# Kernel tuning notes

Hardware: AMD Instinct MI355X
Metric: run time of the kernel (lower is better)

## Reference

```python
import jax, jax.numpy as jnp
import numpy as np
import math

B, N, R = 1024, 50, 1000
N_POIS = 50000
D = 128
K_T = 64
K_D = 64
T_MAX = 10080.0
D_MAX = 200.0
EARTH_RADIUS_KM = 6371.0
DEG2RAD = math.pi / 180.0


def _interp_scalar(table, x):
    # Linear interpolation into 1-D table [K]; x are bin positions in [0, K-1].
    K = table.shape[0]
    x = jnp.clip(x, 0.0, K - 1 - 1e-06)
    k = jnp.floor(x).astype(jnp.int32)
    frac = x - k.astype(x.dtype)
    return (1.0 - frac) * table[k] + frac * table[jnp.minimum(k + 1, K - 1)]


def _haversine_km(lat1, lon1, lat2, lon2):
    dlat = (lat2 - lat1) * DEG2RAD
    dlon = (lon2 - lon1) * DEG2RAD
    a = jnp.sin(dlat / 2) ** 2 + jnp.cos(lat1 * DEG2RAD) * jnp.cos(lat2 * DEG2RAD) * jnp.sin(dlon / 2) ** 2
    a = jnp.clip(a, 0.0, 1.0)
    return EARTH_RADIUS_KM * 2.0 * jnp.arcsin(jnp.sqrt(a))


def setup_inputs() -> dict:
    key = jax.random.key(0)
    ks = jax.random.split(key, 16)
    poi_idx = jax.random.randint(ks[0], (B, N), 0, N_POIS)
    hour_of_week = jax.random.randint(ks[1], (B, N), 0, 169)
    lat = jax.random.uniform(ks[2], (B, N), jnp.float32)  # ~1 degree spread => up to ~150 km pairwise
    lon = jax.random.uniform(ks[3], (B, N), jnp.float32)
    t_min = jax.random.uniform(ks[4], (B, N), jnp.float32) * T_MAX
    region_centroids = jax.random.uniform(ks[5], (R, 2), jnp.float32)
    poi_emb = 0.02 * jax.random.normal(ks[6], (N_POIS + 1, D), jnp.float32)
    poi_emb = poi_emb.at[N_POIS].set(0.0)  # padding row
    time_emb = 0.02 * jax.random.normal(ks[7], (169, D), jnp.float32)
    time_emb = time_emb.at[0].set(0.0)  # padding row
    E_t = 0.1 * jax.random.normal(ks[8], (K_T,), jnp.float32)
    E_d = 0.1 * jax.random.normal(ks[9], (K_D,), jnp.float32)
    E_d_match = 0.1 * jax.random.normal(ks[10], (K_D,), jnp.float32)
    region_emb = 0.02 * jax.random.normal(ks[11], (R, D), jnp.float32)
    Wq = jax.random.normal(ks[12], (D, D), jnp.float32) / math.sqrt(D)
    Wk = jax.random.normal(ks[13], (D, D), jnp.float32) / math.sqrt(D)
    Wv = jax.random.normal(ks[14], (D, D), jnp.float32) / math.sqrt(D)
    return dict(poi_idx=poi_idx, hour_of_week=hour_of_week, lat=lat, lon=lon, t_min=t_min,
                region_centroids=region_centroids, poi_emb=poi_emb, time_emb=time_emb,
                E_t=E_t, E_d=E_d, E_d_match=E_d_match, region_emb=region_emb,
                Wq=Wq, Wk=Wk, Wv=Wv)


def reference(poi_idx, hour_of_week, lat, lon, t_min, region_centroids,
              poi_emb, time_emb, E_t, E_d, E_d_match, region_emb, Wq, Wk, Wv):
    pad_mask = poi_idx < 0  # [B, n]
    poi_safe = jnp.where(pad_mask, N_POIS, poi_idx)
    hour_safe = jnp.where(pad_mask, 0, hour_of_week)
    x = poi_emb[poi_safe] + time_emb[hour_safe]  # [B, n, D]

    # pairwise trajectory intervals [B, n, n]
    dt = jnp.abs(t_min[:, :, None] - t_min[:, None, :])
    dd = _haversine_km(lat[:, :, None], lon[:, :, None], lat[:, None, :], lon[:, None, :])
    valid = (~pad_mask).astype(x.dtype)
    valid_pair = valid[:, :, None] * valid[:, None, :]
    dt = dt * valid_pair
    dd = dd * valid_pair

    # _PairwiseBias: scalar table interpolation bias
    t_bin = jnp.clip(dt, 0.0, T_MAX) / T_MAX * (K_T - 1)
    d_bin = jnp.clip(dd, 0.0, D_MAX) / D_MAX * (K_D - 1)
    bias = _interp_scalar(E_t, t_bin) + _interp_scalar(E_d, d_bin)  # [B, n, n]

    # _SelfAttn (single head, no LN/residual, dropout=0)
    Q = x @ Wq.T
    K_ = x @ Wk.T
    V = x @ Wv.T
    scores = jnp.einsum('bnd,bmd->bnm', Q, K_) / math.sqrt(D) + bias
    scores = jnp.where(pad_mask[:, None, :], -jnp.inf, scores)
    attn = jnp.nan_to_num(jax.nn.softmax(scores, axis=-1), nan=0.0)
    S = attn @ V  # [B, n, D]

    # _MatchingLayer
    cand_lat = region_centroids[:, 0]
    cand_lon = region_centroids[:, 1]
    dd_m = _haversine_km(lat[:, :, None], lon[:, :, None], cand_lat[None, None, :], cand_lon[None, None, :])  # [B, n, R]
    dbin_m = jnp.clip(dd_m, 0.0, D_MAX) / D_MAX * (K_D - 1)
    bias_match = _interp_scalar(E_d_match, dbin_m)
    m_scores = jnp.einsum('bnd,rd->bnr', S, region_emb) / math.sqrt(D) + bias_match
    m_scores = jnp.where(pad_mask[:, :, None], -jnp.inf, m_scores)
    m_attn = jnp.nan_to_num(jax.nn.softmax(m_scores, axis=1), nan=0.0)  # softmax over trajectory dim
    scores_safe = jnp.where(pad_mask[:, :, None], 0.0, m_scores)
    return jnp.sum(m_attn * scores_safe, axis=1)  # [B, R]
```

## Files before the change

### kernel.cpp

```cpp
#include <hip/hip_runtime.h>
#include <hip/hip_bf16.h>
#include <math.h>

constexpr int BB    = 1024;
constexpr int NN    = 50;
constexpr int RR    = 1000;
constexpr int DD    = 128;
constexpr int NPOIS = 50000;
#define DEG2RADF  0.017453292519943295f
#define KHALF     0.008726646259971648f
#define RSQRTD    0.08838834764831845f
#define LOG2E     1.4426950408889634f
#define LN2       0.6931471805599453f
#define DBIN_C0   4013.7373f
#define DBIN_C1   668.95621f
#define TBIN_SC   0.00625f
#define PENAL     -1.0e30f

typedef __attribute__((ext_vector_type(8))) short bfrag8;
typedef __attribute__((ext_vector_type(4))) float f32x4;

__device__ __forceinline__ int swz128(int row, int k) {
    return row * 128 + ((((k) >> 3) ^ (row & 7)) << 3) + (k & 7);
}

__device__ __forceinline__ unsigned short f2bf(float x) {
    union { __hip_bfloat16 h; unsigned short u; } cv;
    cv.h = __float2bfloat16(x);
    return cv.u;
}

__device__ __forceinline__ float exp2_asm(float x) {
    float r;
    asm("v_exp_f32 %0, %1" : "=v"(r) : "v"(x));
    return r;
}

__device__ __forceinline__ float fract_asm(float x) {
    float r;
    asm("v_fract_f32 %0, %1" : "=v"(r) : "v"(x));
    return r;
}

__device__ __forceinline__ float cos_small(float x) {
    float x2 = x * x;
    return 1.0f - 0.5f * x2 + 0.041666667f * x2 * x2;
}

__global__ void prep_mg(const float* __restrict__ Wq, const float* __restrict__ Wk,
                        const float* __restrict__ Wv, const float* __restrict__ Re,
                        unsigned short* __restrict__ Mt, unsigned short* __restrict__ Gp) {
    int k = threadIdx.x;
    if (blockIdx.x < DD) {
        int c = blockIdx.x;
        float s0 = 0.f, s1 = 0.f, s2 = 0.f, s3 = 0.f;
        for (int d = 0; d < DD; d += 4) {
            s0 += Wq[(d + 0) * DD + k] * Wk[(d + 0) * DD + c];
            s1 += Wq[(d + 1) * DD + k] * Wk[(d + 1) * DD + c];
            s2 += Wq[(d + 2) * DD + k] * Wk[(d + 2) * DD + c];
            s3 += Wq[(d + 3) * DD + k] * Wk[(d + 3) * DD + c];
        }
        Mt[c * DD + k] = f2bf((s0 + s1 + s2 + s3) * (RSQRTD * LOG2E));
    } else {
        int r = blockIdx.x - DD;
        float val = 0.f;
        if (r < RR) {
            float s0 = 0.f, s1 = 0.f, s2 = 0.f, s3 = 0.f;
            for (int d = 0; d < DD; d += 4) {
                s0 += Wv[(d + 0) * DD + k] * Re[r * DD + d + 0];
                s1 += Wv[(d + 1) * DD + k] * Re[r * DD + d + 1];
                s2 += Wv[(d + 2) * DD + k] * Re[r * DD + d + 2];
                s3 += Wv[(d + 3) * DD + k] * Re[r * DD + d + 3];
            }
            val = (s0 + s1 + s2 + s3) * (RSQRTD * LOG2E);
        }
        int rt = r >> 6, widr = (r >> 4) & 3, colr = r & 15;
        int ks = k >> 5, quad = (k >> 3) & 3, k7 = k & 7;
        int lane = quad * 16 + colr;
        Gp[((((rt * 16 + widr * 4 + ks) * 64) + lane) << 3) + k7] = f2bf(val);
    }
}

__global__ __launch_bounds__(256, 4) void stan_fused(
    const int* __restrict__ poi_idx, const int* __restrict__ hourw,
    const float* __restrict__ lat, const float* __restrict__ lon,
    const float* __restrict__ tmin,
    const float* __restrict__ poi_emb, const float* __restrict__ time_emb,
    const float* __restrict__ Et_g, const float* __restrict__ Ed_g,
    const float* __restrict__ Em_g,
    const unsigned short* __restrict__ Mtb, const unsigned short* __restrict__ Gp,
    const float* __restrict__ cent, float* __restrict__ out) {
    __shared__ short xs[64 * 128];
    __shared__ union {
        short ys[64 * 128];
        short ps[64 * 64];
        short as_[64 * 128];
    } u2;
    __shared__ float2 Et2[64], Ed2[64], Em2[64];
    __shared__ float4 bnfo[64];
    __shared__ float4 bnfoM[64];
    __shared__ float  jpen[64];
    __shared__ int2   nidx[64];

    const int b = blockIdx.x, tid = threadIdx.x;
    const int wid = tid >> 6, lane = tid & 63;
    const int quad = lane >> 4, colr = lane & 15;

    if (tid < 64) {
        int kk = tid > 62 ? 62 : tid;
        float t0 = Et_g[kk] * LOG2E, t1 = Et_g[kk + 1] * LOG2E;
        float d0 = Ed_g[kk] * LOG2E, d1 = Ed_g[kk + 1] * LOG2E;
        float e0 = Em_g[kk] * LOG2E, e1 = Em_g[kk + 1] * LOG2E;
        Et2[tid] = make_float2(t0, t1 - t0);
        Ed2[tid] = make_float2(d0, d1 - d0);
        Em2[tid] = make_float2(e0, e1 - e0);
        if (tid < NN) {
            int p = poi_idx[b * NN + tid];
            int pd = (p < 0);
            float la = lat[b * NN + tid], lo = lon[b * NN + tid];
            float cs = cos_small(la * DEG2RADF);
            float pen = pd ? PENAL : 0.f;
            nidx[tid] = make_int2(pd ? NPOIS : p, pd ? 0 : hourw[b * NN + tid]);
            bnfo[tid]  = make_float4(la * KHALF, lo * KHALF, cs,
                                     tmin[b * NN + tid] * TBIN_SC);
            bnfoM[tid] = make_float4(la * KHALF, lo * KHALF, cs, pen);
            jpen[tid] = pen;
        } else {
            nidx[tid] = make_int2(NPOIS, 0);
            bnfo[tid]  = make_float4(0.f, 0.f, 1.f, 0.f);
            bnfoM[tid] = make_float4(0.f, 0.f, 1.f, PENAL);
            jpen[tid] = PENAL;
        }
    }
    __syncthreads();

    for (int idx = tid; idx < 64 * 64; idx += 256) {
        int n = idx >> 6, c2 = idx & 63;
        int2 ix = nidx[n];
        float2 pe = ((const float2*)(poi_emb  + (size_t)ix.x * DD))[c2];
        float2 te = ((const float2*)(time_emb + (size_t)ix.y * DD))[c2];
        unsigned pack = (unsigned)f2bf(pe.x + te.x)
                      | ((unsigned)f2bf(pe.y + te.y) << 16);
        ((unsigned*)xs)[n * 64 + (((c2 >> 2) ^ (n & 7)) << 2) + (c2 & 3)] = pack;
    }
    __syncthreads();

    const int q8    = (quad ^ (colr & 3)) * 8;
    const int kx    = (colr & 4) * 8;
    const int xbase = colr * 128 + q8;
    const int xe = xbase + kx, xo = xbase - kx;

    {
        f32x4 accY[2][4];
        #pragma unroll
        for (int ct = 0; ct < 2; ct++)
            #pragma unroll
            for (int mt = 0; mt < 4; mt++) accY[ct][mt] = (f32x4){0.f, 0.f, 0.f, 0.f};
        #pragma unroll
        for (int ks = 0; ks < 4; ks++) {
            const int k0 = ks * 32 + quad * 8;
            const int xoff = ((ks & 1) ? xo : xe) + ks * 32;
            bfrag8 av[4], bv[2];
            #pragma unroll
            for (int mt = 0; mt < 4; mt++)
                av[mt] = *(const bfrag8*)(&xs[xoff + mt * 2048]);
            #pragma unroll
            for (int ct = 0; ct < 2; ct++) {
                int c = wid * 32 + ct * 16 + colr;
                bv[ct] = *(const bfrag8*)(Mtb + (size_t)c * DD + k0);
            }
            #pragma unroll
            for (int ct = 0; ct < 2; ct++)
                #pragma unroll
                for (int mt = 0; mt < 4; mt++)
                    accY[ct][mt] = __builtin_amdgcn_mfma_f32_16x16x32_bf16(
                        av[mt], bv[ct], accY[ct][mt], 0, 0, 0);
        }
        #pragma unroll
        for (int ct = 0; ct < 2; ct++)
            #pragma unroll
            for (int mt = 0; mt < 4; mt++)
                #pragma unroll
                for (int reg = 0; reg < 4; reg++) {
                    int m = mt * 16 + quad * 4 + reg;
                    int c = wid * 32 + ct * 16 + colr;
                    u2.ys[swz128(m, c)] = (short)f2bf(accY[ct][mt][reg]);
                }
    }
    __syncthreads();

    const int i = wid * 16 + colr;
    const int ybase = xbase + wid * 2048;
    const int ye = ybase + kx, yo = ybase - kx;
    f32x4 accS[4];
    #pragma unroll
    for (int mt = 0; mt < 4; mt++) accS[mt] = (f32x4){0.f, 0.f, 0.f, 0.f};
    #pragma unroll
    for (int ks = 0; ks < 4; ks++) {
        const int yoff = ((ks & 1) ? yo : ye) + ks * 32;
        const int xoff = ((ks & 1) ? xo : xe) + ks * 32;
        bfrag8 bv = *(const bfrag8*)(&u2.ys[yoff]);
        #pragma unroll
        for (int mt = 0; mt < 4; mt++) {
            bfrag8 av = *(const bfrag8*)(&xs[xoff + mt * 2048]);
            accS[mt] = __builtin_amdgcn_mfma_f32_16x16x32_bf16(
                av, bv, accS[mt], 0, 0, 0);
        }
    }
    __syncthreads();

    {
        const float4 bi = bnfo[i];
        float sv[14];
        #pragma unroll
        for (int mt = 0; mt < 4; mt++) {
            const int nregs = (mt == 3) ? 2 : 4;
            #pragma unroll
            for (int reg = 0; reg < nregs; reg++) {
                int j = mt * 16 + quad * 4 + reg;
                float4 bj = bnfo[j];
                float tb = fabsf(bi.w - bj.w);
                int   kt = (int)tb;
                float ft = fract_asm(tb);
                float2 et = Et2[kt];
                float bt = fmaf(ft, et.y, et.x);
                float du = bi.x - bj.x, dv = bi.y - bj.y;
                float a = fmaf((bi.z * bj.z) * dv, dv, du * du);
                float x = __builtin_amdgcn_sqrtf(a);
                float db = x * fmaf(a, DBIN_C1, DBIN_C0);
                int   kd = (int)db;
                float fd = fract_asm(db);
                float2 ed = Ed2[kd];
                float bd = fmaf(fd, ed.y, ed.x);
                sv[mt * 4 + reg] = (accS[mt][reg] + bt) + (bd + jpen[j]);
            }
        }
        float l = 0.f;
        #pragma unroll
        for (int t = 0; t < 14; t++) {
            float p = exp2_asm(sv[t]);
            sv[t] = p;
            l += p;
        }
        l += __shfl_xor(l, 16, 64);
        l += __shfl_xor(l, 32, 64);
        float rl = __builtin_amdgcn_rcpf(l);
        #pragma unroll
        for (int mt = 0; mt < 4; mt++)
            #pragma unroll
            for (int rp = 0; rp < 2; rp++) {
                int j0 = mt * 16 + quad * 4 + rp * 2;
                unsigned pack;
                if (mt == 3 && rp == 1) {
                    pack = 0u;
                } else {
                    unsigned lo = f2bf(sv[mt * 4 + rp * 2]     * rl);
                    unsigned hi = f2bf(sv[mt * 4 + rp * 2 + 1] * rl);
                    pack = lo | (hi << 16);
                }
                ((unsigned*)u2.ps)[i * 32 + (((j0 >> 3) ^ (i & 7)) << 2) + ((j0 & 7) >> 1)]
                    = pack;
            }
    }
    __syncthreads();

    {
        f32x4 accZ[2][4];
        #pragma unroll
        for (int nt = 0; nt < 2; nt++)
            #pragma unroll
            for (int mt = 0; mt < 4; mt++) accZ[nt][mt] = (f32x4){0.f, 0.f, 0.f, 0.f};
        union BF { unsigned u[4]; bfrag8 v; };
        const int pbase = colr * 64 + q8;
        const int pe = pbase + kx, po = pbase - kx;
        #pragma unroll
        for (int ks = 0; ks < 2; ks++) {
            const int k0 = ks * 32 + quad * 8;
            const int poff = ((ks & 1) ? po : pe) + ks * 32;
            bfrag8 av[4];
            #pragma unroll
            for (int mt = 0; mt < 4; mt++)
                av[mt] = *(const bfrag8*)(&u2.ps[poff + mt * 1024]);
            BF bvx[2];
            #pragma unroll
            for (int nt = 0; nt < 2; nt++) {
                int d = wid * 32 + nt * 16 + colr;
                #pragma unroll
                for (int t2 = 0; t2 < 4; t2++) {
                    unsigned lo = (unsigned short)xs[swz128(k0 + 2 * t2,     d)];
                    unsigned hi = (unsigned short)xs[swz128(k0 + 2 * t2 + 1, d)];
                    bvx[nt].u[t2] = lo | (hi << 16);
                }
            }
            #pragma unroll
            for (int nt = 0; nt < 2; nt++)
                #pragma unroll
                for (int mt = 0; mt < 4; mt++)
                    accZ[nt][mt] = __builtin_amdgcn_mfma_f32_16x16x32_bf16(
                        av[mt], bvx[nt].v, accZ[nt][mt], 0, 0, 0);
        }
        __syncthreads();
        #pragma unroll
        for (int mt = 0; mt < 4; mt++)
            #pragma unroll
            for (int reg = 0; reg < 4; reg++) {
                int ii = mt * 16 + quad * 4 + reg;
                #pragma unroll
                for (int nt = 0; nt < 2; nt++) {
                    int d = wid * 32 + nt * 16 + colr;
                    float zv = (ii < NN) ? accZ[nt][mt][reg] : 0.f;
                    u2.as_[swz128(ii, d)] = (short)f2bf(zv);
                }
            }
    }
    __syncthreads();

    bfrag8 Af[4][4];
    #pragma unroll
    for (int ks = 0; ks < 4; ks++) {
        const int aoff = ((ks & 1) ? xo : xe) + ks * 32;
        #pragma unroll
        for (int mt = 0; mt < 4; mt++)
            Af[mt][ks] = *(const bfrag8*)(&u2.as_[aoff + mt * 2048]);
    }
    bfrag8 bfv[4];
    #pragma unroll
    for (int ks = 0; ks < 4; ks++)
        bfv[ks] = *(const bfrag8*)(Gp + (size_t)(((wid * 4 + ks) * 64 + lane) << 3));

    const int rL = wid * 16 + colr;

    #pragma unroll 1
    for (int it = 0; it < 16; it++) {
        f32x4 acc[4];
        #pragma unroll
        for (int mt = 0; mt < 4; mt++) acc[mt] = (f32x4){0.f, 0.f, 0.f, 0.f};
        #pragma unroll
        for (int ks = 0; ks < 4; ks++)
            #pragma unroll
            for (int mt = 0; mt < 4; mt++)
                acc[mt] = __builtin_amdgcn_mfma_f32_16x16x32_bf16(
                    Af[mt][ks], bfv[ks], acc[mt], 0, 0, 0);

        {
            const int rtn = (it < 15) ? it + 1 : it;
            #pragma unroll
            for (int ks = 0; ks < 4; ks++)
                bfv[ks] = *(const bfrag8*)(Gp + (size_t)(((rtn * 16 + wid * 4 + ks) * 64 + lane) << 3));
        }

        const int r  = it * 64 + rL;
        const int rc = (r < RR) ? r : (RR - 1);
        float2 cc = ((const float2*)cent)[rc];
        const float rvx = cc.x * KHALF, rvy = cc.y * KHALF;
        const float rvz = cos_small(cc.x * DEG2RADF);

        float l = 0.f, aw = 0.f;
        #pragma unroll
        for (int mt = 0; mt < 4; mt++) {
            const int nregs = (mt == 3) ? 2 : 4;
            #pragma unroll
            for (int reg = 0; reg < nregs; reg++) {
                int n = mt * 16 + quad * 4 + reg;
                float4 bn = bnfoM[n];
                float du = bn.x - rvx, dv = bn.y - rvy;
                float a = fmaf((bn.z * rvz) * dv, dv, du * du);
                float x = __builtin_amdgcn_sqrtf(a);
                float db = x * fmaf(a, DBIN_C1, DBIN_C0);
                int   kd = (int)db;
                float fd = fract_asm(db);
                float2 ed = Em2[kd];
                float bias = fmaf(fd, ed.y, ed.x);
                float sc = (acc[mt][reg] + bias) + bn.w;
                float p = exp2_asm(sc);
                l += p;
                aw = fmaf(p, sc, aw);
            }
        }
        l  += __shfl_xor(l, 16, 64); aw += __shfl_xor(aw, 16, 64);
        l  += __shfl_xor(l, 32, 64); aw += __shfl_xor(aw, 32, 64);
        if (quad == 0 && r < RR)
            out[(size_t)b * RR + r] = aw * __builtin_amdgcn_rcpf(l) * LN2;
    }
}

extern "C" void kernel_launch(void* const* d_in, const int* in_sizes, int n_in,
                              void* d_out, int out_size, void* d_ws, size_t ws_size,
                              hipStream_t stream) {
    const int*   poi_idx  = (const int*)d_in[0];
    const int*   hourw    = (const int*)d_in[1];
    const float* lat      = (const float*)d_in[2];
    const float* lon      = (const float*)d_in[3];
    const float* tmin     = (const float*)d_in[4];
    const float* cent     = (const float*)d_in[5];
    const float* poi_emb  = (const float*)d_in[6];
    const float* time_emb = (const float*)d_in[7];
    const float* E_t      = (const float*)d_in[8];
    const float* E_d      = (const float*)d_in[9];
    const float* E_dm     = (const float*)d_in[10];
    const float* Remb     = (const float*)d_in[11];
    const float* Wq       = (const float*)d_in[12];
    const float* Wk       = (const float*)d_in[13];
    const float* Wv       = (const float*)d_in[14];
    float* out            = (float*)d_out;

    unsigned short* Mtb = (unsigned short*)d_ws;
    unsigned short* Gpb = Mtb + DD * DD;

    prep_mg<<<dim3(DD + 1024), DD, 0, stream>>>(Wq, Wk, Wv, Remb, Mtb, Gpb);
    stan_fused<<<dim3(BB), 256, 0, stream>>>(poi_idx, hourw, lat, lon, tmin,
                                             poi_emb, time_emb, E_t, E_d, E_dm,
                                             Mtb, Gpb, cent, out);
}
```

Before: 152.4 us.

## Process two region tiles per iteration and reload A fragments from LDS

```diff
diff --git a/kernel.cpp b/kernel.cpp
--- a/kernel.cpp
+++ b/kernel.cpp
@@ -315,72 +315,76 @@
     }
     __syncthreads();
 
-    bfrag8 Af[4][4];
+    bfrag8 bf0[4], bf1[4];
     #pragma unroll
     for (int ks = 0; ks < 4; ks++) {
-        const int aoff = ((ks & 1) ? xo : xe) + ks * 32;
-        #pragma unroll
-        for (int mt = 0; mt < 4; mt++)
-            Af[mt][ks] = *(const bfrag8*)(&u2.as_[aoff + mt * 2048]);
-    }
-    bfrag8 bfv[4];
-    #pragma unroll
-    for (int ks = 0; ks < 4; ks++)
-        bfv[ks] = *(const bfrag8*)(Gp + (size_t)(((wid * 4 + ks) * 64 + lane) << 3));
+        bf0[ks] = *(const bfrag8*)(Gp + (size_t)(((      wid * 4 + ks) * 64 + lane) << 3));
+        bf1[ks] = *(const bfrag8*)(Gp + (size_t)(((16  + wid * 4 + ks) * 64 + lane) << 3));
+    }
 
     const int rL = wid * 16 + colr;
 
     #pragma unroll 1
-    for (int it = 0; it < 16; it++) {
-        f32x4 acc[4];
-        #pragma unroll
-        for (int mt = 0; mt < 4; mt++) acc[mt] = (f32x4){0.f, 0.f, 0.f, 0.f};
-        #pragma unroll
-        for (int ks = 0; ks < 4; ks++)
-            #pragma unroll
-            for (int mt = 0; mt < 4; mt++)
-                acc[mt] = __builtin_amdgcn_mfma_f32_16x16x32_bf16(
-                    Af[mt][ks], bfv[ks], acc[mt], 0, 0, 0);
-
+    for (int ot = 0; ot < 8; ot++) {
+        f32x4 acc0[4], acc1[4];
+        #pragma unroll
+        for (int mt = 0; mt < 4; mt++) {
+            acc0[mt] = (f32x4){0.f, 0.f, 0.f, 0.f};
+            acc1[mt] = (f32x4){0.f, 0.f, 0.f, 0.f};
+        }
+        #pragma unroll
+        for (int ks = 0; ks < 4; ks++) {
+            const int aoff = ((ks & 1) ? xo : xe) + ks * 32;
+            #pragma unroll
+            for (int mt = 0; mt < 4; mt++) {
+                bfrag8 af = *(const bfrag8*)(&u2.as_[aoff + mt * 2048]);
+                acc0[mt] = __builtin_amdgcn_mfma_f32_16x16x32_bf16(af, bf0[ks], acc0[mt], 0, 0, 0);
+                acc1[mt] = __builtin_amdgcn_mfma_f32_16x16x32_bf16(af, bf1[ks], acc1[mt], 0, 0, 0);
+            }
+        }
         {
-            const int rtn = (it < 15) ? it + 1 : it;
-            #pragma unroll
-            for (int ks = 0; ks < 4; ks++)
-                bfv[ks] = *(const bfrag8*)(Gp + (size_t)(((rtn * 16 + wid * 4 + ks) * 64 + lane) << 3));
-        }
-
-        const int r  = it * 64 + rL;
-        const int rc = (r < RR) ? r : (RR - 1);
-        float2 cc = ((const float2*)cent)[rc];
-        const float rvx = cc.x * KHALF, rvy = cc.y * KHALF;
-        const float rvz = cos_small(cc.x * DEG2RADF);
-
-        float l = 0.f, aw = 0.f;
-        #pragma unroll
-        for (int mt = 0; mt < 4; mt++) {
-            const int nregs = (mt == 3) ? 2 : 4;
-            #pragma unroll
-            for (int reg = 0; reg < nregs; reg++) {
-                int n = mt * 16 + quad * 4 + reg;
-                float4 bn = bnfoM[n];
-                float du = bn.x - rvx, dv = bn.y - rvy;
-                float a = fmaf((bn.z * rvz) * dv, dv, du * du);
-                float x = __builtin_amdgcn_sqrtf(a);
-                float db = x * fmaf(a, DBIN_C1, DBIN_C0);
-                int   kd = (int)db;
-                float fd = fract_asm(db);
-                float2 ed = Em2[kd];
-                float bias = fmaf(fd, ed.y, ed.x);
-                float sc = (acc[mt][reg] + bias) + bn.w;
-                float p = exp2_asm(sc);
-                l += p;
-                aw = fmaf(p, sc, aw);
-            }
-        }
-        l  += __shfl_xor(l, 16, 64); aw += __shfl_xor(aw, 16, 64);
-        l  += __shfl_xor(l, 32, 64); aw += __shfl_xor(aw, 32, 64);
-        if (quad == 0 && r < RR)
-            out[(size_t)b * RR + r] = aw * __builtin_amdgcn_rcpf(l) * LN2;
+            const int rn0 = (ot < 7) ? 2 * ot + 2 : 14;
+            #pragma unroll
+            for (int ks = 0; ks < 4; ks++) {
+                bf0[ks] = *(const bfrag8*)(Gp + (size_t)((( rn0      * 16 + wid * 4 + ks) * 64 + lane) << 3));
+                bf1[ks] = *(const bfrag8*)(Gp + (size_t)((((rn0 + 1) * 16 + wid * 4 + ks) * 64 + lane) << 3));
+            }
+        }
+        #pragma unroll
+        for (int half = 0; half < 2; half++) {
+            const int r  = (2 * ot + half) * 64 + rL;
+            const int rc = (r < RR) ? r : (RR - 1);
+            float2 cc = ((const float2*)cent)[rc];
+            const float rvx = cc.x * KHALF, rvy = cc.y * KHALF;
+            const float rvz = cos_small(cc.x * DEG2RADF);
+            float l = 0.f, aw = 0.f;
+            #pragma unroll
+            for (int mt = 0; mt < 4; mt++) {
+                const int nregs = (mt == 3) ? 2 : 4;
+                #pragma unroll
+                for (int reg = 0; reg < nregs; reg++) {
+                    int n = mt * 16 + quad * 4 + reg;
+                    float4 bn = bnfoM[n];
+                    float du = bn.x - rvx, dv = bn.y - rvy;
+                    float a = fmaf((bn.z * rvz) * dv, dv, du * du);
+                    float x = __builtin_amdgcn_sqrtf(a);
+                    float db = x * fmaf(a, DBIN_C1, DBIN_C0);
+                    int   kd = (int)db;
+                    float fd = fract_asm(db);
+                    float2 ed = Em2[kd];
+                    float bias = fmaf(fd, ed.y, ed.x);
+                    float av_ = half ? acc1[mt][reg] : acc0[mt][reg];
+                    float sc = (av_ + bias) + bn.w;
+                    float p = exp2_asm(sc);
+                    l += p;
+                    aw = fmaf(p, sc, aw);
+                }
+            }
+            l  += __shfl_xor(l, 16, 64); aw += __shfl_xor(aw, 16, 64);
+            l  += __shfl_xor(l, 32, 64); aw += __shfl_xor(aw, 32, 64);
+            if (quad == 0 && r < RR)
+                out[(size_t)b * RR + r] = aw * __builtin_amdgcn_rcpf(l) * LN2;
+        }
     }
 }
 
```

Measured after the change: 217.9 us. 1.43x slower.
